# Optimization experiments

Hardware: AMD Instinct MI355X
Metric: run time of the kernel (lower is better)

## Reference

```python
import jax, jax.numpy as jnp
import numpy as np

L = 4        # num_hidden_layers
D = 1024     # dmodel (== inputsize)
FF = 4096    # dff
H = 16       # num_heads
DH = D // H  # head dim
B, S = 2, 2048
EPS = 1e-6


def _layer_norm(x, g, b):
    m = jnp.mean(x, axis=-1, keepdims=True)
    v = jnp.mean(jnp.square(x - m), axis=-1, keepdims=True)
    return (x - m) * jax.lax.rsqrt(v + EPS) * g + b


def setup_inputs() -> dict:
    key = jax.random.key(0)
    ks = jax.random.split(key, 16)
    sd = 0.02
    inp = {
        "hidden_states": jax.random.normal(ks[0], (B, S, D), jnp.float32),
        # stacked per-layer params (weights stored [in, out])
        "Wq": jax.random.normal(ks[1], (L, D, D), jnp.float32) * sd,
        "bq": jnp.zeros((L, D), jnp.float32),
        "Wk": jax.random.normal(ks[2], (L, D, D), jnp.float32) * sd,
        "bk": jnp.zeros((L, D), jnp.float32),
        "Wv": jax.random.normal(ks[3], (L, D, D), jnp.float32) * sd,
        "bv": jnp.zeros((L, D), jnp.float32),
        "Wp": jax.random.normal(ks[4], (L, D, D), jnp.float32) * sd,
        "bp": jnp.zeros((L, D), jnp.float32),
        "ln1_g": jnp.ones((L, D), jnp.float32),
        "ln1_b": jnp.zeros((L, D), jnp.float32),
        "W1": jax.random.normal(ks[5], (L, D, FF), jnp.float32) * sd,
        "b1": jnp.zeros((L, FF), jnp.float32),
        "W2": jax.random.normal(ks[6], (L, FF, D), jnp.float32) * sd,
        "b2": jnp.zeros((L, D), jnp.float32),
        "ln2_g": jnp.ones((L, D), jnp.float32),
        "ln2_b": jnp.zeros((L, D), jnp.float32),
    }
    return inp


def reference(hidden_states, Wq, bq, Wk, bk, Wv, bv, Wp, bp, ln1_g, ln1_b,
              W1, b1, W2, b2, ln2_g, ln2_b):
    x = hidden_states
    scale = 1.0 / jnp.sqrt(jnp.asarray(DH, x.dtype))
    for l in range(L):
        # --- AttentionIn ---
        q = (x @ Wq[l] + bq[l]).reshape(B, S, H, DH)
        k = (x @ Wk[l] + bk[l]).reshape(B, S, H, DH)
        v = (x @ Wv[l] + bv[l]).reshape(B, S, H, DH)
        scores = jnp.einsum('bqhd,bkhd->bhqk', q, k) * scale
        probs = jax.nn.softmax(scores, axis=-1)
        ctx = jnp.einsum('bhqk,bkhd->bqhd', probs, v).reshape(B, S, D)
        ctx = ctx @ Wp[l] + bp[l]
        x = _layer_norm(ctx + x, ln1_g[l], ln1_b[l])
        # --- AttentionOutput (FFN with residual + LN); dropout=0 ---
        h = jax.nn.relu(x @ W1[l] + b1[l]) @ W2[l] + b2[l]
        x = _layer_norm(h + x, ln2_g[l], ln2_b[l])
    return x
```

## Files before the change

kernel.cpp:

```cpp
#include <hip/hip_runtime.h>

#define D_  1024
#define FF_ 4096
#define H_  16
#define DH_ 64
#define B_  2
#define S_  2048
#define M_  4096

typedef __attribute__((ext_vector_type(8))) __bf16 bf16x8;
typedef __attribute__((ext_vector_type(4))) short short4v;
typedef __attribute__((ext_vector_type(4))) float floatx4;

typedef __attribute__((address_space(1))) unsigned int as1_uint;
typedef __attribute__((address_space(3))) unsigned int as3_uint;

__device__ __forceinline__ unsigned short f2bf(float f) {
    unsigned u = __float_as_uint(f);
    u += 0x7FFFu + ((u >> 16) & 1u);
    return (unsigned short)(u >> 16);
}

__device__ __forceinline__ int packbf(float a, float b) {
    return (int)((__float_as_uint(a) >> 16) | (__float_as_uint(b) & 0xFFFF0000u));
}

__device__ __forceinline__ void gl_lds16(const void* g, void* l) {
    __builtin_amdgcn_global_load_lds((as1_uint*)(unsigned long long)g,
                                     (as3_uint*)l, 16, 0, 0);
}

struct TDesc { const float* src; unsigned short* dst; int K; int N; int ntx; };
struct TPack { TDesc d[6]; int cum[7]; };

__global__ __launch_bounds__(256) void transpose_cvt_batch(TPack p)
{
    __shared__ float tile[32][33];
    int bid = blockIdx.x;
    int seg = 0;
    while (bid >= p.cum[seg + 1]) ++seg;
    const TDesc d = p.d[seg];
    const int t = bid - p.cum[seg];
    const int n0 = (t % d.ntx) * 32, k0 = (t / d.ntx) * 32;
    const int tx = threadIdx.x, ty = threadIdx.y;
#pragma unroll
    for (int i = 0; i < 32; i += 8)
        tile[ty + i][tx] = d.src[(size_t)(k0 + ty + i) * d.N + n0 + tx];
    __syncthreads();
#pragma unroll
    for (int i = 0; i < 32; i += 8)
        d.dst[(size_t)(n0 + ty + i) * d.K + k0 + tx] = f2bf(tile[tx][ty + i]);
}

__global__ __launch_bounds__(256) void transpose_v(
    const unsigned short* __restrict__ V, unsigned short* __restrict__ VT)
{
    __shared__ unsigned short t[64][72];
    const int bh = blockIdx.y, s0 = blockIdx.x * 64;
    const int tid = threadIdx.x;
#pragma unroll
    for (int i = 0; i < 2; i++) {
        int u = tid + i * 256;
        int s = u >> 3, dc = u & 7;
        uint4 v = *(const uint4*)(V + ((size_t)bh * S_ + s0 + s) * DH_ + dc * 8);
        *(uint4*)&t[s][dc * 8] = v;
    }
    __syncthreads();
    const int dh = tid >> 2, sc = (tid & 3) * 16;
    unsigned v[16];
#pragma unroll
    for (int j = 0; j < 16; j++) v[j] = t[sc + j][dh];
    uint4 o0, o1;
    o0.x = v[0] | (v[1] << 16);  o0.y = v[2] | (v[3] << 16);
    o0.z = v[4] | (v[5] << 16);  o0.w = v[6] | (v[7] << 16);
    o1.x = v[8] | (v[9] << 16);  o1.y = v[10] | (v[11] << 16);
    o1.z = v[12] | (v[13] << 16); o1.w = v[14] | (v[15] << 16);
    unsigned short* dst = VT + ((size_t)bh * DH_ + dh) * S_ + s0 + sc;
    *(uint4*)dst = o0;
    *(uint4*)(dst + 8) = o1;
}

__global__ __launch_bounds__(256) void cvt_x0(
    const float* __restrict__ in, float* __restrict__ xf, unsigned short* __restrict__ xh)
{
    int i = blockIdx.x * 256 + threadIdx.x;
    float4 v = ((const float4*)in)[i];
    ((float4*)xf)[i] = v;
    uint2 h;
    h.x = (unsigned)f2bf(v.x) | ((unsigned)f2bf(v.y) << 16);
    h.y = (unsigned)f2bf(v.z) | ((unsigned)f2bf(v.w) << 16);
    ((uint2*)xh)[i] = h;
}

template <int EPI, int KSPLIT>
__global__ __launch_bounds__(256) void gemm128(
    const unsigned short* __restrict__ A, const unsigned short* __restrict__ BT,
    int M, int N, int K,
    const float* __restrict__ b0, const float* __restrict__ b1, const float* __restrict__ b2,
    float* __restrict__ outF, float* __restrict__ outF2, unsigned short* __restrict__ outH,
    unsigned short* __restrict__ qO, unsigned short* __restrict__ kO, unsigned short* __restrict__ vO)
{
    __shared__ __align__(16) unsigned short As[128 * 64];
    __shared__ __align__(16) unsigned short Bs[128 * 64];

    const int tid = threadIdx.x;
    const int m0 = blockIdx.y * 128, n0 = blockIdx.x * 128;
    const int kchunk = K / KSPLIT;
    const int kbase = (KSPLIT > 1) ? (int)blockIdx.z * kchunk : 0;
    const int lane = tid & 63, wv = tid >> 6;
    const int wm = wv & 1, wn = wv >> 1;
    const int cl = lane & 15, quad = lane >> 4;

    const int srow = tid >> 3, sslot = tid & 7;
    const int schk = sslot ^ (srow & 7);
    const unsigned short* gA = A  + (size_t)(m0 + srow) * K + kbase + schk * 8;
    const unsigned short* gB = BT + (size_t)(n0 + srow) * K + kbase + schk * 8;

    floatx4 acc[4][4];
#pragma unroll
    for (int i = 0; i < 4; i++)
#pragma unroll
        for (int j = 0; j < 4; j++) acc[i][j] = (floatx4){0.f, 0.f, 0.f, 0.f};

    for (int kt = 0; kt < kchunk; kt += 64) {
#pragma unroll
        for (int i = 0; i < 4; i++) {
            gl_lds16(gA + (size_t)(32 * i) * K + kt, &As[(size_t)(tid + 256 * i) * 8]);
            gl_lds16(gB + (size_t)(32 * i) * K + kt, &Bs[(size_t)(tid + 256 * i) * 8]);
        }
        __syncthreads();

        bf16x8 av[4][2], bv[4][2];
#pragma unroll
        for (int mi = 0; mi < 4; mi++) {
            const int row = wm * 64 + mi * 16 + cl;
#pragma unroll
            for (int ks = 0; ks < 2; ks++)
                av[mi][ks] = *(const bf16x8*)&As[row * 64 + (((ks * 4 + quad) ^ (cl & 7)) * 8)];
        }
#pragma unroll
        for (int ni = 0; ni < 4; ni++) {
            const int row = wn * 64 + ni * 16 + cl;
#pragma unroll
            for (int ks = 0; ks < 2; ks++)
                bv[ni][ks] = *(const bf16x8*)&Bs[row * 64 + (((ks * 4 + quad) ^ (cl & 7)) * 8)];
        }
#pragma unroll
        for (int mi = 0; mi < 4; mi++)
#pragma unroll
            for (int ni = 0; ni < 4; ni++) {
                acc[mi][ni] = __builtin_amdgcn_mfma_f32_16x16x32_bf16(
                    av[mi][0], bv[ni][0], acc[mi][ni], 0, 0, 0);
                acc[mi][ni] = __builtin_amdgcn_mfma_f32_16x16x32_bf16(
                    av[mi][1], bv[ni][1], acc[mi][ni], 0, 0, 0);
            }
        __syncthreads();
    }

    float* outFz = nullptr;
    if (EPI == 0) {
        const int z = (KSPLIT > 1) ? (int)blockIdx.z : 0;
        outFz = ((z < 2) ? outF : outF2) + (size_t)(z & 1) * M * N;
    }
#pragma unroll
    for (int mi = 0; mi < 4; mi++) {
#pragma unroll
        for (int ni = 0; ni < 4; ni++) {
            const int c = n0 + wn * 64 + ni * 16 + cl;
#pragma unroll
            for (int r = 0; r < 4; r++) {
                const int rr = m0 + wm * 64 + mi * 16 + quad * 4 + r;
                float v = acc[mi][ni][r];
                if (EPI == 0) {
                    outFz[(size_t)rr * N + c] = v;
                } else if (EPI == 1) {
                    float t = v + b0[c];
                    outH[(size_t)rr * N + c] = f2bf(t > 0.f ? t : 0.f);
                } else {
                    const int kind = c >> 10, cc = c & 1023;
                    const float* bp = (kind == 0) ? b0 : (kind == 1) ? b1 : b2;
                    float t = v + bp[cc];
                    if (kind == 0) t *= 0.18033688f;
                    const int h = cc >> 6, dh = cc & 63;
                    const int bb = rr >> 11, s = rr & 2047;
                    unsigned short* dst = (kind == 0) ? qO : (kind == 1) ? kO : vO;
                    dst[((size_t)(bb * H_ + h) * S_ + s) * DH_ + dh] = f2bf(t);
                }
            }
        }
    }
}

__global__ __launch_bounds__(256) void attn_kernel(
    const unsigned short* __restrict__ Qg, const unsigned short* __restrict__ Kg,
    const unsigned short* __restrict__ VTg, unsigned short* __restrict__ ctx)
{
    __shared__ __align__(16) unsigned short Ks[2][64 * 64];
    __shared__ __align__(16) unsigned short Vs[2][64 * 64];

    const int tid = threadIdx.x, lane = tid & 63, wv = tid >> 6;
    const int cl = lane & 15, quad = lane >> 4;

    const int lin = blockIdx.x;
    const int idx = lin >> 3;
    const int bh  = (lin & 7) * 4 + (idx & 3);
    const int qt  = idx >> 2;
    const int qrow = qt * 64 + wv * 16 + cl;
    const size_t bhS = (size_t)bh * S_;

    bf16x8 aq[2];
#pragma unroll
    for (int ks = 0; ks < 2; ks++)
        aq[ks] = *(const bf16x8*)(Qg + (bhS + qrow) * DH_ + ks * 32 + quad * 8);

    floatx4 O[4];
#pragma unroll
    for (int i = 0; i < 4; i++) O[i] = (floatx4){0.f, 0.f, 0.f, 0.f};
    float l_cur = 0.f;

    const int g0 = tid, g1 = tid + 256;
    const int r_0 = g0 >> 3, c_0 = (g0 & 7) ^ (r_0 & 7);
    const int r_1 = g1 >> 3, c_1 = (g1 & 7) ^ (r_1 & 7);
    const unsigned short* kp0 = Kg + (bhS + r_0) * DH_ + c_0 * 8;
    const unsigned short* kp1 = Kg + (bhS + r_1) * DH_ + c_1 * 8;
    const unsigned short* vp0 = VTg + ((size_t)bh * DH_ + r_0) * S_ + c_0 * 8;
    const unsigned short* vp1 = VTg + ((size_t)bh * DH_ + r_1) * S_ + c_1 * 8;

    int koff0[4], koff1[4], voff[4][4];
#pragma unroll
    for (int mi = 0; mi < 4; mi++) {
        const int row = mi * 16 + cl;
        koff0[mi] = (row * 8 + (quad       ^ (cl & 7))) * 8;
        koff1[mi] = (row * 8 + ((4 + quad) ^ (cl & 7))) * 8;
#pragma unroll
        for (int c16 = 0; c16 < 4; c16++) {
            const int slot = (c16 * 2 + (quad >> 1)) ^ (cl & 7);
            voff[c16][mi] = (row * 8 + slot) * 8 + (quad & 1) * 4;
        }
    }

    gl_lds16(kp0, &Ks[0][(size_t)g0 * 8]);
    gl_lds16(kp1, &Ks[0][(size_t)g1 * 8]);
    gl_lds16(vp0, &Vs[0][(size_t)g0 * 8]);
    gl_lds16(vp1, &Vs[0][(size_t)g1 * 8]);

    for (int t = 0; t < S_ / 64; t++) {
        __syncthreads();
        if (t < S_ / 64 - 1) {
            const int k0n = (t + 1) * 64;
            const int bn = (t + 1) & 1;
            gl_lds16(kp0 + (size_t)k0n * DH_, &Ks[bn][(size_t)g0 * 8]);
            gl_lds16(kp1 + (size_t)k0n * DH_, &Ks[bn][(size_t)g1 * 8]);
            gl_lds16(vp0 + k0n, &Vs[bn][(size_t)g0 * 8]);
            gl_lds16(vp1 + k0n, &Vs[bn][(size_t)g1 * 8]);
        }
        const unsigned short* Kb = Ks[t & 1];
        const unsigned short* Vb = Vs[t & 1];

        floatx4 sc[4];
#pragma unroll
        for (int mi = 0; mi < 4; mi++) {
            bf16x8 kf0 = *(const bf16x8*)&Kb[koff0[mi]];
            bf16x8 kf1 = *(const bf16x8*)&Kb[koff1[mi]];
            floatx4 z = (floatx4){0.f, 0.f, 0.f, 0.f};
            z = __builtin_amdgcn_mfma_f32_16x16x32_bf16(kf0, aq[0], z, 0, 0, 0);
            sc[mi] = __builtin_amdgcn_mfma_f32_16x16x32_bf16(kf1, aq[1], z, 0, 0, 0);
        }

        int pk[4][2];
#pragma unroll
        for (int mi = 0; mi < 4; mi++) {
            float p0 = __builtin_amdgcn_exp2f(sc[mi][0]);
            float p1 = __builtin_amdgcn_exp2f(sc[mi][1]);
            float p2 = __builtin_amdgcn_exp2f(sc[mi][2]);
            float p3 = __builtin_amdgcn_exp2f(sc[mi][3]);
            l_cur += (p0 + p1) + (p2 + p3);
            pk[mi][0] = packbf(p0, p1);
            pk[mi][1] = packbf(p2, p3);
        }

#pragma unroll
        for (int c16 = 0; c16 < 4; c16++) {
            union { int i[2]; short4v s; } pb;
            pb.i[0] = pk[c16][0];
            pb.i[1] = pk[c16][1];
#pragma unroll
            for (int mi2 = 0; mi2 < 4; mi2++) {
                short4v va = *(const short4v*)&Vb[voff[c16][mi2]];
                O[mi2] = __builtin_amdgcn_mfma_f32_16x16x16bf16_1k(va, pb.s, O[mi2], 0, 0, 0);
            }
        }
    }

    l_cur += __shfl_xor(l_cur, 16);
    l_cur += __shfl_xor(l_cur, 32);

    const float invl = 1.f / l_cur;
    const int b = bh >> 4, h = bh & 15;
    unsigned short* cp = ctx + ((size_t)(b * S_ + qrow)) * D_ + h * DH_ + quad * 4;
#pragma unroll
    for (int mi2 = 0; mi2 < 4; mi2++) {
        unsigned short w[4];
#pragma unroll
        for (int r = 0; r < 4; r++) w[r] = f2bf(O[mi2][r] * invl);
        unsigned o0 = (unsigned)w[0] | ((unsigned)w[1] << 16);
        unsigned o1 = (unsigned)w[2] | ((unsigned)w[3] << 16);
        uint2 ov; ov.x = o0; ov.y = o1;
        *(uint2*)(cp + mi2 * 16) = ov;
    }
}

template <int NP>
__global__ __launch_bounds__(256) void ln_kernel(
    const float* __restrict__ t, const float* __restrict__ t2,
    const float* __restrict__ bias, const float* __restrict__ xr,
    const float* __restrict__ g, const float* __restrict__ b,
    float* __restrict__ xf, unsigned short* __restrict__ xh, float* __restrict__ extra)
{
    const int row = blockIdx.x, tid = threadIdx.x;
    float4 a = ((const float4*)(t + (size_t)row * D_))[tid];
#pragma unroll
    for (int p = 1; p < NP; p++) {
        const float* src = ((p < 2) ? t : t2) + (size_t)(p & 1) * M_ * D_;
        const float4 ap = ((const float4*)(src + (size_t)row * D_))[tid];
        a.x += ap.x; a.y += ap.y; a.z += ap.z; a.w += ap.w;
    }
    const float4 bs = ((const float4*)bias)[tid];
    const float4 c = ((const float4*)(xr + (size_t)row * D_))[tid];
    float4 y;
    y.x = a.x + bs.x + c.x; y.y = a.y + bs.y + c.y;
    y.z = a.z + bs.z + c.z; y.w = a.w + bs.w + c.w;
    float s  = y.x + y.y + y.z + y.w;
    float sq = y.x * y.x + y.y * y.y + y.z * y.z + y.w * y.w;
#pragma unroll
    for (int off = 1; off < 64; off <<= 1) {
        s  += __shfl_xor(s, off);
        sq += __shfl_xor(sq, off);
    }
    __shared__ float red[8];
    const int wv = tid >> 6, lane = tid & 63;
    if (lane == 0) { red[wv] = s; red[4 + wv] = sq; }
    __syncthreads();
    s  = red[0] + red[1] + red[2] + red[3];
    sq = red[4] + red[5] + red[6] + red[7];
    const float mean = s * (1.f / D_);
    const float var  = sq * (1.f / D_) - mean * mean;
    const float ri   = rsqrtf(var + 1e-6f);
    const float4 gg = ((const float4*)g)[tid];
    const float4 bb = ((const float4*)b)[tid];
    float4 o;
    o.x = (y.x - mean) * ri * gg.x + bb.x;
    o.y = (y.y - mean) * ri * gg.y + bb.y;
    o.z = (y.z - mean) * ri * gg.z + bb.z;
    o.w = (y.w - mean) * ri * gg.w + bb.w;
    ((float4*)(xf + (size_t)row * D_))[tid] = o;
    uint2 h;
    h.x = (unsigned)f2bf(o.x) | ((unsigned)f2bf(o.y) << 16);
    h.y = (unsigned)f2bf(o.z) | ((unsigned)f2bf(o.w) << 16);
    ((uint2*)(xh + (size_t)row * D_))[tid] = h;
    if (extra) ((float4*)(extra + (size_t)row * D_))[tid] = o;
}

extern "C" void kernel_launch(void* const* d_in, const int* in_sizes, int n_in,
                              void* d_out, int out_size, void* d_ws, size_t ws_size,
                              hipStream_t stream)
{
    const float* hs  = (const float*)d_in[0];
    const float* Wq  = (const float*)d_in[1];
    const float* bq  = (const float*)d_in[2];
    const float* Wk  = (const float*)d_in[3];
    const float* bk  = (const float*)d_in[4];
    const float* Wv  = (const float*)d_in[5];
    const float* bv  = (const float*)d_in[6];
    const float* Wp  = (const float*)d_in[7];
    const float* bp  = (const float*)d_in[8];
    const float* g1  = (const float*)d_in[9];
    const float* be1 = (const float*)d_in[10];
    const float* W1  = (const float*)d_in[11];
    const float* b1  = (const float*)d_in[12];
    const float* W2  = (const float*)d_in[13];
    const float* b2  = (const float*)d_in[14];
    const float* g2  = (const float*)d_in[15];
    const float* be2 = (const float*)d_in[16];

    char* w = (char*)d_ws;
    auto alloc = [&](size_t bytes) { char* p = w; w += (bytes + 255) & ~(size_t)255; return p; };
    unsigned short* wqkvT = (unsigned short*)alloc(3072ull * 1024 * 2);
    unsigned short* wpT   = (unsigned short*)alloc(1024ull * 1024 * 2);
    unsigned short* w1T   = (unsigned short*)alloc(4096ull * 1024 * 2);
    unsigned short* w2T   = (unsigned short*)alloc(1024ull * 4096 * 2);
    float*          xf    = (float*)alloc(4096ull * 1024 * 4);
    unsigned short* xh    = (unsigned short*)alloc(4096ull * 1024 * 2);
    unsigned short* qb_   = (unsigned short*)alloc(4096ull * 1024 * 2);
    unsigned short* kb_   = (unsigned short*)alloc(4096ull * 1024 * 2);
    unsigned short* vb_   = (unsigned short*)alloc(4096ull * 1024 * 2);
    unsigned short* ctx   = (unsigned short*)alloc(4096ull * 1024 * 2);
    float*          part  = (float*)alloc(2ull * 4096 * 1024 * 4);
    unsigned short* hh    = (unsigned short*)alloc(4096ull * 4096 * 2);
    unsigned short* vtb   = hh;
    float*          part2 = (float*)qb_;

    const dim3 blk(256);
    const dim3 tb(32, 8);

    cvt_x0<<<4096, blk, 0, stream>>>(hs, xf, xh);

    for (int l = 0; l < 4; l++) {
        TPack tp;
        tp.d[0] = { Wq + (size_t)l * D_ * D_,  wqkvT,                   D_,  D_,  32 };
        tp.d[1] = { Wk + (size_t)l * D_ * D_,  wqkvT + 1024 * 1024,     D_,  D_,  32 };
        tp.d[2] = { Wv + (size_t)l * D_ * D_,  wqkvT + 2 * 1024 * 1024, D_,  D_,  32 };
        tp.d[3] = { Wp + (size_t)l * D_ * D_,  wpT,                     D_,  D_,  32 };
        tp.d[4] = { W1 + (size_t)l * D_ * FF_, w1T,                     D_,  FF_, 128 };
        tp.d[5] = { W2 + (size_t)l * FF_ * D_, w2T,                     FF_, D_,  32 };
        tp.cum[0] = 0;    tp.cum[1] = 1024; tp.cum[2] = 2048; tp.cum[3] = 3072;
        tp.cum[4] = 4096; tp.cum[5] = 8192; tp.cum[6] = 12288;
        transpose_cvt_batch<<<12288, tb, 0, stream>>>(tp);

        gemm128<2, 1><<<dim3(24, 32), blk, 0, stream>>>(xh, wqkvT, M_, 3 * D_, D_,
            bq + l * D_, bk + l * D_, bv + l * D_,
            nullptr, nullptr, nullptr, qb_, kb_, vb_);

        transpose_v<<<dim3(32, 32), blk, 0, stream>>>(vb_, vtb);

        attn_kernel<<<1024, blk, 0, stream>>>(qb_, kb_, vtb, ctx);

        gemm128<0, 2><<<dim3(8, 32, 2), blk, 0, stream>>>(ctx, wpT, M_, D_, D_,
            nullptr, nullptr, nullptr, part, part, nullptr, nullptr, nullptr, nullptr);

        ln_kernel<2><<<4096, blk, 0, stream>>>(part, part, bp + l * D_, xf,
            g1 + l * D_, be1 + l * D_, xf, xh, nullptr);

        gemm128<1, 1><<<dim3(32, 32), blk, 0, stream>>>(xh, w1T, M_, FF_, D_,
            b1 + l * FF_, nullptr, nullptr, nullptr, nullptr, hh, nullptr, nullptr, nullptr);

        gemm128<0, 4><<<dim3(8, 32, 4), blk, 0, stream>>>(hh, w2T, M_, D_, FF_,
            nullptr, nullptr, nullptr, part, part2, nullptr, nullptr, nullptr, nullptr);

        ln_kernel<4><<<4096, blk, 0, stream>>>(part, part2, b2 + l * D_, xf,
            g2 + l * D_, be2 + l * D_, xf, xh,
            (l == 3) ? (float*)d_out : nullptr);
    }
}
```

Before: 1.240 ms.

## Store split-K partials in bf16 and use 128-key single-buffered attention tiles

Split-K GEMM partial sums are now written as bf16 rather than fp32, and the layernorm kernel reads and sums the bf16 partials. This halves partial-sum write and read traffic, at the cost of precision in the residual-branch sums. The attention kernel also swaps its double-buffered 64-key K/V tiles for single-buffered 128-key tiles with a barrier after each load. That halves the number of loop iterations but gives up the overlap between loading and computing.

Measured after the change: 1.219 ms. Within noise of the previous version (-1.7%).

```diff
diff --git a/kernel.cpp b/kernel.cpp
--- a/kernel.cpp
+++ b/kernel.cpp
@@ -97,7 +97,7 @@
     const unsigned short* __restrict__ A, const unsigned short* __restrict__ BT,
     int M, int N, int K,
     const float* __restrict__ b0, const float* __restrict__ b1, const float* __restrict__ b2,
-    float* __restrict__ outF, float* __restrict__ outF2, unsigned short* __restrict__ outH,
+    unsigned short* __restrict__ outH,
     unsigned short* __restrict__ qO, unsigned short* __restrict__ kO, unsigned short* __restrict__ vO)
 {
     __shared__ __align__(16) unsigned short As[128 * 64];
@@ -157,11 +157,8 @@
         __syncthreads();
     }
 
-    float* outFz = nullptr;
-    if (EPI == 0) {
-        const int z = (KSPLIT > 1) ? (int)blockIdx.z : 0;
-        outFz = ((z < 2) ? outF : outF2) + (size_t)(z & 1) * M * N;
-    }
+    unsigned short* outHz = outH;
+    if (EPI == 0 && KSPLIT > 1) outHz = outH + (size_t)blockIdx.z * M * N;
 #pragma unroll
     for (int mi = 0; mi < 4; mi++) {
 #pragma unroll
@@ -172,7 +169,7 @@
                 const int rr = m0 + wm * 64 + mi * 16 + quad * 4 + r;
                 float v = acc[mi][ni][r];
                 if (EPI == 0) {
-                    outFz[(size_t)rr * N + c] = v;
+                    outHz[(size_t)rr * N + c] = f2bf(v);
                 } else if (EPI == 1) {
                     float t = v + b0[c];
                     outH[(size_t)rr * N + c] = f2bf(t > 0.f ? t : 0.f);
@@ -195,8 +192,8 @@
     const unsigned short* __restrict__ Qg, const unsigned short* __restrict__ Kg,
     const unsigned short* __restrict__ VTg, unsigned short* __restrict__ ctx)
 {
-    __shared__ __align__(16) unsigned short Ks[2][64 * 64];
-    __shared__ __align__(16) unsigned short Vs[2][64 * 64];
+    __shared__ __align__(16) unsigned short Ks[128 * 64];
+    __shared__ __align__(16) unsigned short Vs[64 * 128];
 
     const int tid = threadIdx.x, lane = tid & 63, wv = tid >> 6;
     const int cl = lane & 15, quad = lane >> 4;
@@ -218,58 +215,56 @@
     for (int i = 0; i < 4; i++) O[i] = (floatx4){0.f, 0.f, 0.f, 0.f};
     float l_cur = 0.f;
 
-    const int g0 = tid, g1 = tid + 256;
-    const int r_0 = g0 >> 3, c_0 = (g0 & 7) ^ (r_0 & 7);
-    const int r_1 = g1 >> 3, c_1 = (g1 & 7) ^ (r_1 & 7);
-    const unsigned short* kp0 = Kg + (bhS + r_0) * DH_ + c_0 * 8;
-    const unsigned short* kp1 = Kg + (bhS + r_1) * DH_ + c_1 * 8;
-    const unsigned short* vp0 = VTg + ((size_t)bh * DH_ + r_0) * S_ + c_0 * 8;
-    const unsigned short* vp1 = VTg + ((size_t)bh * DH_ + r_1) * S_ + c_1 * 8;
-
-    int koff0[4], koff1[4], voff[4][4];
-#pragma unroll
-    for (int mi = 0; mi < 4; mi++) {
+    const unsigned short* kp[4];
+    const unsigned short* vp[4];
+#pragma unroll
+    for (int i = 0; i < 4; i++) {
+        const int g = tid + 256 * i;
+        const int kr = g >> 3, ksl = g & 7, kch = ksl ^ (kr & 7);
+        kp[i] = Kg + (bhS + kr) * DH_ + kch * 8;
+        const int vr = g >> 4, vsl = g & 15, vch = vsl ^ (vr & 7);
+        vp[i] = VTg + ((size_t)bh * DH_ + vr) * S_ + vch * 8;
+    }
+
+    int koff0[8], koff1[8], voff[8][4];
+#pragma unroll
+    for (int mi = 0; mi < 8; mi++) {
         const int row = mi * 16 + cl;
         koff0[mi] = (row * 8 + (quad       ^ (cl & 7))) * 8;
         koff1[mi] = (row * 8 + ((4 + quad) ^ (cl & 7))) * 8;
-#pragma unroll
-        for (int c16 = 0; c16 < 4; c16++) {
+    }
+#pragma unroll
+    for (int c16 = 0; c16 < 8; c16++)
+#pragma unroll
+        for (int mi2 = 0; mi2 < 4; mi2++) {
+            const int row = mi2 * 16 + cl;
             const int slot = (c16 * 2 + (quad >> 1)) ^ (cl & 7);
-            voff[c16][mi] = (row * 8 + slot) * 8 + (quad & 1) * 4;
-        }
-    }
-
-    gl_lds16(kp0, &Ks[0][(size_t)g0 * 8]);
-    gl_lds16(kp1, &Ks[0][(size_t)g1 * 8]);
-    gl_lds16(vp0, &Vs[0][(size_t)g0 * 8]);
-    gl_lds16(vp1, &Vs[0][(size_t)g1 * 8]);
-
-    for (int t = 0; t < S_ / 64; t++) {
+            voff[c16][mi2] = (row * 16 + slot) * 8 + (quad & 1) * 4;
+        }
+
+    for (int k0 = 0; k0 < S_; k0 += 128) {
         __syncthreads();
-        if (t < S_ / 64 - 1) {
-            const int k0n = (t + 1) * 64;
-            const int bn = (t + 1) & 1;
-            gl_lds16(kp0 + (size_t)k0n * DH_, &Ks[bn][(size_t)g0 * 8]);
-            gl_lds16(kp1 + (size_t)k0n * DH_, &Ks[bn][(size_t)g1 * 8]);
-            gl_lds16(vp0 + k0n, &Vs[bn][(size_t)g0 * 8]);
-            gl_lds16(vp1 + k0n, &Vs[bn][(size_t)g1 * 8]);
-        }
-        const unsigned short* Kb = Ks[t & 1];
-        const unsigned short* Vb = Vs[t & 1];
-
-        floatx4 sc[4];
-#pragma unroll
-        for (int mi = 0; mi < 4; mi++) {
-            bf16x8 kf0 = *(const bf16x8*)&Kb[koff0[mi]];
-            bf16x8 kf1 = *(const bf16x8*)&Kb[koff1[mi]];
+#pragma unroll
+        for (int i = 0; i < 4; i++) {
+            const int g = tid + 256 * i;
+            gl_lds16(kp[i] + (size_t)k0 * DH_, &Ks[(size_t)g * 8]);
+            gl_lds16(vp[i] + k0,               &Vs[(size_t)g * 8]);
+        }
+        __syncthreads();
+
+        floatx4 sc[8];
+#pragma unroll
+        for (int mi = 0; mi < 8; mi++) {
+            bf16x8 kf0 = *(const bf16x8*)&Ks[koff0[mi]];
+            bf16x8 kf1 = *(const bf16x8*)&Ks[koff1[mi]];
             floatx4 z = (floatx4){0.f, 0.f, 0.f, 0.f};
             z = __builtin_amdgcn_mfma_f32_16x16x32_bf16(kf0, aq[0], z, 0, 0, 0);
             sc[mi] = __builtin_amdgcn_mfma_f32_16x16x32_bf16(kf1, aq[1], z, 0, 0, 0);
         }
 
-        int pk[4][2];
-#pragma unroll
-        for (int mi = 0; mi < 4; mi++) {
+        int pk[8][2];
+#pragma unroll
+        for (int mi = 0; mi < 8; mi++) {
             float p0 = __builtin_amdgcn_exp2f(sc[mi][0]);
             float p1 = __builtin_amdgcn_exp2f(sc[mi][1]);
             float p2 = __builtin_amdgcn_exp2f(sc[mi][2]);
@@ -280,13 +275,13 @@
         }
 
 #pragma unroll
-        for (int c16 = 0; c16 < 4; c16++) {
+        for (int c16 = 0; c16 < 8; c16++) {
             union { int i[2]; short4v s; } pb;
             pb.i[0] = pk[c16][0];
             pb.i[1] = pk[c16][1];
 #pragma unroll
             for (int mi2 = 0; mi2 < 4; mi2++) {
-                short4v va = *(const short4v*)&Vb[voff[c16][mi2]];
+                short4v va = *(const short4v*)&Vs[voff[c16][mi2]];
                 O[mi2] = __builtin_amdgcn_mfma_f32_16x16x16bf16_1k(va, pb.s, O[mi2], 0, 0, 0);
             }
         }
@@ -312,18 +307,20 @@
 
 template <int NP>
 __global__ __launch_bounds__(256) void ln_kernel(
-    const float* __restrict__ t, const float* __restrict__ t2,
-    const float* __restrict__ bias, const float* __restrict__ xr,
+    const unsigned short* __restrict__ ph, const float* __restrict__ bias,
+    const float* __restrict__ xr,
     const float* __restrict__ g, const float* __restrict__ b,
     float* __restrict__ xf, unsigned short* __restrict__ xh, float* __restrict__ extra)
 {
     const int row = blockIdx.x, tid = threadIdx.x;
-    float4 a = ((const float4*)(t + (size_t)row * D_))[tid];
-#pragma unroll
-    for (int p = 1; p < NP; p++) {
-        const float* src = ((p < 2) ? t : t2) + (size_t)(p & 1) * M_ * D_;
-        const float4 ap = ((const float4*)(src + (size_t)row * D_))[tid];
-        a.x += ap.x; a.y += ap.y; a.z += ap.z; a.w += ap.w;
+    float4 a = {0.f, 0.f, 0.f, 0.f};
+#pragma unroll
+    for (int p = 0; p < NP; p++) {
+        const uint2 hv = ((const uint2*)(ph + (size_t)p * M_ * D_ + (size_t)row * D_))[tid];
+        a.x += __uint_as_float(hv.x << 16);
+        a.y += __uint_as_float(hv.x & 0xFFFF0000u);
+        a.z += __uint_as_float(hv.y << 16);
+        a.w += __uint_as_float(hv.y & 0xFFFF0000u);
     }
     const float4 bs = ((const float4*)bias)[tid];
     const float4 c = ((const float4*)(xr + (size_t)row * D_))[tid];
@@ -395,10 +392,9 @@
     unsigned short* kb_   = (unsigned short*)alloc(4096ull * 1024 * 2);
     unsigned short* vb_   = (unsigned short*)alloc(4096ull * 1024 * 2);
     unsigned short* ctx   = (unsigned short*)alloc(4096ull * 1024 * 2);
-    float*          part  = (float*)alloc(2ull * 4096 * 1024 * 4);
+    unsigned short* part  = (unsigned short*)alloc(4ull * 4096 * 1024 * 2);
     unsigned short* hh    = (unsigned short*)alloc(4096ull * 4096 * 2);
     unsigned short* vtb   = hh;
-    float*          part2 = (float*)qb_;
 
     const dim3 blk(256);
     const dim3 tb(32, 8);
@@ -419,25 +415,25 @@
 
         gemm128<2, 1><<<dim3(24, 32), blk, 0, stream>>>(xh, wqkvT, M_, 3 * D_, D_,
             bq + l * D_, bk + l * D_, bv + l * D_,
-            nullptr, nullptr, nullptr, qb_, kb_, vb_);
+            nullptr, qb_, kb_, vb_);
 
         transpose_v<<<dim3(32, 32), blk, 0, stream>>>(vb_, vtb);
 
         attn_kernel<<<1024, blk, 0, stream>>>(qb_, kb_, vtb, ctx);
 
         gemm128<0, 2><<<dim3(8, 32, 2), blk, 0, stream>>>(ctx, wpT, M_, D_, D_,
-            nullptr, nullptr, nullptr, part, part, nullptr, nullptr, nullptr, nullptr);
-
-        ln_kernel<2><<<4096, blk, 0, stream>>>(part, part, bp + l * D_, xf,
+            nullptr, nullptr, nullptr, part, nullptr, nullptr, nullptr);
+
+        ln_kernel<2><<<4096, blk, 0, stream>>>(part, bp + l * D_, xf,
             g1 + l * D_, be1 + l * D_, xf, xh, nullptr);
 
         gemm128<1, 1><<<dim3(32, 32), blk, 0, stream>>>(xh, w1T, M_, FF_, D_,
-            b1 + l * FF_, nullptr, nullptr, nullptr, nullptr, hh, nullptr, nullptr, nullptr);
+            b1 + l * FF_, nullptr, nullptr, hh, nullptr, nullptr, nullptr);
 
         gemm128<0, 4><<<dim3(8, 32, 4), blk, 0, stream>>>(hh, w2T, M_, D_, FF_,
-            nullptr, nullptr, nullptr, part, part2, nullptr, nullptr, nullptr, nullptr);
-
-        ln_kernel<4><<<4096, blk, 0, stream>>>(part, part2, b2 + l * D_, xf,
+            nullptr, nullptr, nullptr, part, nullptr, nullptr, nullptr);
+
+        ln_kernel<4><<<4096, blk, 0, stream>>>(part, b2 + l * D_, xf,
             g2 + l * D_, be2 + l * D_, xf, xh,
             (l == 3) ? (float*)d_out : nullptr);
     }
```
